# Kernel optimization log

Hardware: AMD Instinct MI355X
Metric: run time of the kernel (lower is better)

Reference implementation:

```python
import jax, jax.numpy as jnp
import numpy as np

B, N, E = 4, 4096, 65536
HID, F_N, F_E, ROUNDS = 128, 32, 16, 3


def setup_inputs() -> dict:
    key = jax.random.key(0)
    ks = jax.random.split(key, 32)
    p = lambda k, shape: 0.02 * jax.random.normal(k, shape, dtype=jnp.float32)
    inp = {
        "nodes": jax.random.normal(ks[0], (B, N, F_N), dtype=jnp.float32),
        "edge_feat": jax.random.normal(ks[1], (B, E, F_E), dtype=jnp.float32),
        "edges": jax.random.randint(ks[2], (B, E, 2), 0, N).astype(jnp.int64),
        "node_mask": jnp.ones((B, N), dtype=bool),
        "edge_mask": jnp.ones((B, E), dtype=bool),
        # projections (stored as (in, out))
        "W_node": p(ks[3], (F_N, HID)),
        "W_edge": p(ks[4], (F_E, HID)),
        "marker": p(ks[5], (HID,)),
        # per-round MLP weights, stacked on leading rounds dim
        "eW1": p(ks[6], (ROUNDS, 3 * HID, HID)),
        "eb1": jnp.zeros((ROUNDS, HID), jnp.float32),
        "eW2": p(ks[7], (ROUNDS, HID, HID)),
        "eb2": jnp.zeros((ROUNDS, HID), jnp.float32),
        "nW1": p(ks[8], (ROUNDS, 2 * HID, HID)),
        "nb1": jnp.zeros((ROUNDS, HID), jnp.float32),
        "nW2": p(ks[9], (ROUNDS, HID, HID)),
        "nb2": jnp.zeros((ROUNDS, HID), jnp.float32),
    }
    return inp


def reference(nodes, edge_feat, edges, node_mask, edge_mask,
              W_node, W_edge, marker, eW1, eb1, eW2, eb2, nW1, nb1, nW2, nb2):
    b, n, _ = nodes.shape
    h = nodes @ W_node                       # (B,N,H)
    ef = edge_feat @ W_edge                  # (B,E,H)
    src = jnp.clip(edges[..., 0], 0, n - 1)  # (B,E)
    dst = jnp.clip(edges[..., 1], 0, n - 1)
    bidx = jnp.arange(b)[:, None]            # (B,1) for batched gather/scatter
    em = edge_mask.astype(h.dtype)[..., None]
    nm = node_mask.astype(h.dtype)[..., None]
    for r in range(ROUNDS):
        h_src = h[bidx, src]                 # (B,E,H) gather
        h_dst = h[bidx, dst]
        cat = jnp.concatenate([h_src, h_dst, ef], axis=-1)   # (B,E,3H)
        msg = jax.nn.silu(cat @ eW1[r] + eb1[r]) @ eW2[r] + eb2[r]
        msg = msg * em
        agg = jnp.zeros_like(h).at[bidx, dst].add(msg)       # scatter-add to nodes
        cat_node = jnp.concatenate([h, agg], axis=-1)        # (B,N,2H)
        upd = jax.nn.silu(cat_node @ nW1[r] + nb1[r]) @ nW2[r] + nb2[r]
        h = (h + upd) * nm
    marker_tok = jnp.broadcast_to(marker[None, None, :], (b, 1, HID))
    return jnp.concatenate([marker_tok, h], axis=1)          # (B,1+N,H)
```

## Files before the change

kernel.cpp:

```cpp
#include <hip/hip_runtime.h>
#include <hip/hip_bf16.h>
#include <cstdint>
#include <cstddef>

#define BB 4
#define NN 4096
#define EE 65536
#define HID 128
#define FN 32
#define FE 16
#define NROUNDS 3

#define XP 168
#define XNP 264
#define PP 136
#define YPITCH 136

typedef __attribute__((ext_vector_type(8))) short short8;
typedef __attribute__((ext_vector_type(4))) float f32x4;
typedef unsigned int uint_t;

__device__ __forceinline__ size_t hrow(int b, int n) {
    return ((size_t)b * (NN + 1) + 1 + n) * HID;
}

__device__ __forceinline__ short f2bf(float f) {
    __hip_bfloat16 h = __float2bfloat16(f);
    return *reinterpret_cast<short*>(&h);
}

__device__ __forceinline__ float bf2f(short s) {
    union { uint32_t u; float f; } v;
    v.u = ((uint32_t)(unsigned short)s) << 16;
    return v.f;
}

__device__ __forceinline__ float bflo(uint_t u) {
    union { uint_t u; float f; } v; v.u = u << 16; return v.f;
}
__device__ __forceinline__ float bfhi(uint_t u) {
    union { uint_t u; float f; } v; v.u = u & 0xFFFF0000u; return v.f;
}

__device__ __forceinline__ float silu(float x) {
    return x * __builtin_amdgcn_rcpf(1.0f + __expf(-x));
}

__device__ __forceinline__ int clipn(int x) {
    return x < 0 ? 0 : (x > NN - 1 ? NN - 1 : x);
}

__global__ void proj_nodes_kernel(const float* __restrict__ nodes,
                                  const float* __restrict__ Wn,
                                  float* __restrict__ hbuf,
                                  short* __restrict__ hbf,
                                  const float* __restrict__ marker,
                                  const float* __restrict__ We,
                                  const float* __restrict__ eW1,
                                  const float* __restrict__ eW2,
                                  const float* __restrict__ nW1,
                                  float* __restrict__ Wec,
                                  float* __restrict__ F,
                                  uint_t* __restrict__ cnt,
                                  uint_t* __restrict__ cntm) {
    __shared__ float nd[8][FN];
    int t = threadIdx.x;
    int row0 = blockIdx.x * 8;

    if (blockIdx.x < 4) {
        hbuf[((size_t)blockIdx.x * (NN + 1)) * HID + t] = marker[t];
    } else if (blockIdx.x < 68) {
        int base = (blockIdx.x - 4) * 256 + t * 2;
        cnt[base] = 0u;  cnt[base + 1] = 0u;
        cntm[base] = 0u; cntm[base + 1] = 0u;
    } else if (blockIdx.x < 116) {
        int lb = blockIdx.x - 68; int r = lb >> 4; int i = lb & 15;
        const float* w1 = eW1 + ((size_t)r * 384 + 256) * HID;
        float acc = 0.f;
        for (int k = 0; k < HID; ++k)
            acc += We[i * HID + k] * w1[k * HID + t];
        Wec[((size_t)r * 16 + i) * HID + t] = acc;
    } else if (blockIdx.x < 500) {
        int lb = blockIdx.x - 116; int r = lb >> 7; int k = lb & 127;
        const float* w2r = eW2 + ((size_t)r * HID + k) * HID;
        const float* n1r = nW1 + ((size_t)r * 256 + 128) * HID;
        float acc = 0.f;
        for (int j = 0; j < HID; ++j)
            acc += w2r[j] * n1r[j * HID + t];
        F[((size_t)r * HID + k) * HID + t] = acc;
    }

    for (int i = 0; i < 2; ++i) {
        int idx = i * 128 + t; int r = idx >> 5; int c = idx & 31;
        nd[r][c] = nodes[(size_t)(row0 + r) * FN + c];
    }
    __syncthreads();
    float acc[8] = {0.f,0.f,0.f,0.f,0.f,0.f,0.f,0.f};
    #pragma unroll
    for (int k = 0; k < FN; ++k) {
        float w = Wn[k * HID + t];
        #pragma unroll
        for (int r = 0; r < 8; ++r) acc[r] += nd[r][k] * w;
    }
    #pragma unroll
    for (int r = 0; r < 8; ++r) {
        int row = row0 + r; int b = row >> 12; int n = row & (NN - 1);
        hbuf[hrow(b, n) + t] = acc[r];
        hbf[(size_t)row * HID + t] = f2bf(acc[r]);
    }
}

__device__ __forceinline__ void pack_generic(const float* __restrict__ W,
                                             short* __restrict__ P,
                                             int KT, size_t rstrideW,
                                             int lb, int lane) {
    int nt = lb & 7;
    int kt = (lb >> 3) % KT;
    int r  = lb / (8 * KT);
    const float* Wr = W + (size_t)r * rstrideW;
    int n  = nt * 16 + (lane & 15);
    int k0 = kt * 32 + (lane >> 4) * 8;
    short v[8];
    #pragma unroll
    for (int i = 0; i < 8; ++i) v[i] = f2bf(Wr[(size_t)(k0 + i) * HID + n]);
    size_t idx = (((size_t)(r * KT + kt) * 8 + nt) * 64 + lane) * 8;
    *(uint4*)&P[idx] = *(uint4*)v;
}

__global__ void pack_all_kernel(const float* __restrict__ eW1,
                                const float* __restrict__ Wec,
                                const float* __restrict__ F,
                                const float* __restrict__ nW1,
                                const float* __restrict__ nW2,
                                const float* __restrict__ eb2,
                                short* __restrict__ W1p,
                                short* __restrict__ eYp,
                                short* __restrict__ nW1p,
                                short* __restrict__ nW2p,
                                float* __restrict__ vecb) {
    int lane = threadIdx.x;
    int bid = blockIdx.x;
    if (bid < 120) {
        const int KT = 5;
        int nt = bid & 7; int kt = (bid >> 3) % KT; int r = bid / (8 * KT);
        int n  = nt * 16 + (lane & 15);
        int k0 = kt * 32 + (lane >> 4) * 8;
        short v[8];
        #pragma unroll
        for (int i = 0; i < 8; ++i) {
            int k = k0 + i;
            float x;
            if (k < 128)      x = eW1[((size_t)r * 384 + k) * HID + n];
            else if (k < 144) x = Wec[((size_t)r * 16 + (k - 128)) * HID + n];
            else              x = 0.f;
            v[i] = f2bf(x);
        }
        size_t idx = (((size_t)(r * KT + kt) * 8 + nt) * 64 + lane) * 8;
        *(uint4*)&W1p[idx] = *(uint4*)v;
    } else if (bid < 216) {
        pack_generic(eW1 + (size_t)128 * HID, eYp, 4, (size_t)384 * HID,
                     bid - 120, lane);
    } else if (bid < 408) {
        const int KT = 8;
        int lb = bid - 216;
        int nt = lb & 7; int kt = (lb >> 3) % KT; int r = lb / (8 * KT);
        int n  = nt * 16 + (lane & 15);
        int k0 = kt * 32 + (lane >> 4) * 8;
        short v[8];
        #pragma unroll
        for (int i = 0; i < 8; ++i) {
            int k = k0 + i;
            float x;
            if (k < 128) x = nW1[((size_t)r * 256 + k) * HID + n];
            else         x = F[((size_t)r * HID + (k - 128)) * HID + n];
            v[i] = f2bf(x);
        }
        size_t idx = (((size_t)(r * KT + kt) * 8 + nt) * 64 + lane) * 8;
        *(uint4*)&nW1p[idx] = *(uint4*)v;
    } else if (bid < 504) {
        pack_generic(nW2, nW2p, 4, (size_t)HID * HID, bid - 408, lane);
    } else {
        int idx = (bid - 504) * 64 + lane;
        int r = idx >> 7; int col = idx & 127;
        const float* n1r = nW1 + ((size_t)r * 256 + 128) * HID;
        float acc = 0.f;
        for (int j = 0; j < HID; ++j)
            acc += eb2[r * HID + j] * n1r[j * HID + col];
        vecb[r * HID + col] = acc;
    }
}

__global__ void hist_kernel(const int* __restrict__ edges,
                            uint_t* __restrict__ cnt) {
    int i = blockIdx.x * 256 + threadIdx.x;
    int b = i >> 16;
    int2 pr = *(const int2*)&edges[(size_t)i * 2];
    int d = clipn(pr.y);
    atomicAdd(&cnt[b * NN + d], 1u);
}

__global__ void scan_kernel(const uint_t* __restrict__ cnt,
                            uint_t* __restrict__ cursor) {
    __shared__ uint_t ps[256];
    int t = threadIdx.x;
    const uint4* c4 = (const uint4*)cnt + (size_t)t * 16;
    uint4 v[16];
    uint_t s = 0;
    #pragma unroll
    for (int i = 0; i < 16; ++i) {
        v[i] = c4[i];
        s += v[i].x + v[i].y + v[i].z + v[i].w;
    }
    ps[t] = s;
    __syncthreads();
    for (int off = 1; off < 256; off <<= 1) {
        uint_t x = (t >= off) ? ps[t - off] : 0u;
        __syncthreads();
        ps[t] += x;
        __syncthreads();
    }
    uint_t run = ps[t] - s;
    uint4* o4 = (uint4*)cursor + (size_t)t * 16;
    #pragma unroll
    for (int i = 0; i < 16; ++i) {
        uint4 o;
        o.x = run;
        o.y = o.x + v[i].x;
        o.z = o.y + v[i].y;
        o.w = o.z + v[i].z;
        run = o.w + v[i].w;
        o4[i] = o;
    }
}

__global__ void scatter_permute_kernel(const int* __restrict__ edges,
                                       const int* __restrict__ emask,
                                       const float* __restrict__ edge_feat,
                                       uint_t* __restrict__ cursor,
                                       uint_t* __restrict__ meta,
                                       short* __restrict__ efs,
                                       uint_t* __restrict__ cntm) {
    int i = blockIdx.x * 256 + threadIdx.x;
    int b = i >> 16;
    int2 pr = *(const int2*)&edges[(size_t)i * 2];
    int s = clipn(pr.x), d = clipn(pr.y);
    uint_t mk = emask[i] ? 1u : 0u;
    if (mk) atomicAdd(&cntm[b * NN + d], 1u);
    uint_t p = atomicAdd(&cursor[b * NN + d], 1u);
    meta[p] = (uint_t)s | ((uint_t)d << 12) | (mk << 24);
    const float* src = edge_feat + (size_t)i * FE;
    short v[16];
    #pragma unroll
    for (int k = 0; k < 16; ++k) v[k] = f2bf(src[k]);
    *(uint4*)(efs + (size_t)p * FE)     = *(uint4*)v;
    *(uint4*)(efs + (size_t)p * FE + 8) = *(uint4*)(v + 8);
}

__global__ __launch_bounds__(256, 6)
void proj_y_kernel(const short* __restrict__ hbf,
                   const short* __restrict__ Wp,
                   const float* __restrict__ b1,
                   short* __restrict__ Y,
                   float* __restrict__ S) {
    __shared__ short X[16 * YPITCH];
    int t = threadIdx.x;
    int row0 = blockIdx.x * 16;

    #pragma unroll
    for (int i = 0; i < 2; ++i) {
        int c = i * 256 + t;
        *(float4*)(S + (size_t)row0 * HID + c * 4) =
            make_float4(0.f, 0.f, 0.f, 0.f);
    }
    {
        int e = t >> 4; int s = t & 15;
        uint4 v = *(const uint4*)(hbf + (size_t)(row0 + e) * HID + s * 8);
        *(uint4*)((char*)X + e * (YPITCH * 2) + s * 16) = v;
    }
    __syncthreads();

    int lane = t & 63;
    int w    = t >> 6;
    int n0 = w * 32;
    int lr = lane & 15;
    int lg = lane >> 4;

    f32x4 acc[2];
    #pragma unroll
    for (int nf = 0; nf < 2; ++nf) {
        float bv = b1[n0 + nf * 16 + lr];
        acc[nf] = (f32x4){bv, bv, bv, bv};
    }
    const char* Xb = (const char*)X;
    for (int kt = 0; kt < 4; ++kt) {
        short8 a = *(const short8*)(Xb + lr * (YPITCH * 2)
                                       + (kt * 32 + lg * 8) * 2);
        const short* wp = Wp + (((size_t)kt * 8 + (n0 >> 4)) * 64 + lane) * 8;
        #pragma unroll
        for (int nf = 0; nf < 2; ++nf) {
            short8 bf = *(const short8*)(wp + (size_t)nf * 64 * 8);
            acc[nf] = __builtin_amdgcn_mfma_f32_16x16x32_bf16(a, bf, acc[nf], 0, 0, 0);
        }
    }
    #pragma unroll
    for (int r = 0; r < 4; ++r) {
        int row = lg * 4 + r;
        #pragma unroll
        for (int nf = 0; nf < 2; ++nf)
            Y[(size_t)(row0 + row) * HID + n0 + nf * 16 + lr]
                = f2bf(acc[nf][r]);
    }
}

__global__ __launch_bounds__(256, 6)
void edge_mfma_csr_kernel(const short* __restrict__ hbf,
                          const short* __restrict__ efs,
                          const uint_t* __restrict__ meta,
                          const short* __restrict__ Y,
                          const short* __restrict__ W1p,
                          float* __restrict__ S) {
    __shared__ short X[64 * XP];
    __shared__ int sdst[64];
    __shared__ float smf[64];
    __shared__ unsigned short segs[65];
    __shared__ int nseg;
    short* Pl = X;

    int t = threadIdx.x;
    int p0 = blockIdx.x * 64;
    int b  = p0 >> 16;

    if (t < 64) {
        uint_t m = meta[p0 + t];
        sdst[t] = (int)((m >> 12) & 0xFFFu);
        smf[t]  = (m >> 24) ? 1.f : 0.f;
        uint_t pm = __shfl_up(m, 1);
        int flag = (t == 0) || (((m ^ pm) & 0x00FFF000u) != 0u);
        unsigned long long mask = __ballot(flag);
        int rank = __popcll(mask & ((1ull << t) - 1ull));
        if (flag) segs[rank] = (unsigned short)t;
        if (t == 0) {
            int ns = __popcll(mask);
            nseg = ns;
            segs[ns] = 64;
        }
    }
    __syncthreads();

    #pragma unroll
    for (int i = 0; i < 4; ++i) {
        int c = i * 256 + t; int e = c >> 4; int s = c & 15;
        int src = (int)(meta[p0 + e] & 0xFFFu);
        uint4 v = *(const uint4*)(hbf + ((size_t)b * NN + src) * HID + s * 8);
        *(uint4*)((char*)X + e * (XP * 2) + s * 16) = v;
    }
    if (t < 128) {
        int e = t >> 1; int s = t & 1;
        uint4 v = *(const uint4*)(efs + (size_t)(p0 + e) * FE + s * 8);
        *(uint4*)((char*)X + e * (XP * 2) + 256 + s * 16) = v;
        *(uint4*)((char*)X + e * (XP * 2) + 288 + s * 16) = make_uint4(0,0,0,0);
    }

    int lane = t & 63;
    int w    = t >> 6;
    int m0 = (w & 1) * 32;
    int n0 = (w >> 1) * 64;
    int lr = lane & 15;
    int lg = lane >> 4;

    f32x4 acc[2][4];
    #pragma unroll
    for (int mf = 0; mf < 2; ++mf)
        #pragma unroll
        for (int r = 0; r < 4; ++r) {
            int row = m0 + mf * 16 + lg * 4 + r;
            const short* yp = Y + ((size_t)b * NN + sdst[row]) * HID + n0 + lr;
            #pragma unroll
            for (int nf = 0; nf < 4; ++nf)
                acc[mf][nf][r] = bf2f(yp[nf * 16]);
        }
    __syncthreads();

    const char* Xb = (const char*)X;
    for (int kt = 0; kt < 5; ++kt) {
        short8 a[2];
        #pragma unroll
        for (int mf = 0; mf < 2; ++mf)
            a[mf] = *(const short8*)(Xb + (m0 + mf * 16 + lr) * (XP * 2)
                                        + (kt * 32 + lg * 8) * 2);
        const short* wp = W1p + (((size_t)kt * 8 + (n0 >> 4)) * 64 + lane) * 8;
        #pragma unroll
        for (int nf = 0; nf < 4; ++nf) {
            short8 bf = *(const short8*)(wp + (size_t)nf * 64 * 8);
            #pragma unroll
            for (int mf = 0; mf < 2; ++mf)
                acc[mf][nf] = __builtin_amdgcn_mfma_f32_16x16x32_bf16(
                    a[mf], bf, acc[mf][nf], 0, 0, 0);
        }
    }
    __syncthreads();

    #pragma unroll
    for (int mf = 0; mf < 2; ++mf)
        #pragma unroll
        for (int nf = 0; nf < 4; ++nf)
            #pragma unroll
            for (int r = 0; r < 4; ++r) {
                int row = m0 + mf * 16 + lg * 4 + r;
                int col = n0 + nf * 16 + lr;
                Pl[row * PP + col] = f2bf(smf[row] * silu(acc[mf][nf][r]));
            }
    __syncthreads();

    {
        int ns = nseg;
        for (int task = t; task < (ns << 6); task += 256) {
            int s  = task >> 6;
            int c2 = (task & 63) * 2;
            int r0 = segs[s], r1 = segs[s + 1];
            float run0 = 0.f, run1 = 0.f;
            for (int r = r0; r < r1; ++r) {
                uint_t pr = *(const uint_t*)&Pl[r * PP + c2];
                run0 += bflo(pr);
                run1 += bfhi(pr);
            }
            float* ap = &S[((size_t)b * NN + sdst[r0]) * HID + c2];
            atomicAdd(ap,     run0);
            atomicAdd(ap + 1, run1);
        }
    }
}

__global__ __launch_bounds__(256, 6)
void node_mfma_kernel(const short* __restrict__ hbf_in,
                      const float* __restrict__ S,
                      const uint_t* __restrict__ cntm,
                      const float* __restrict__ vec,
                      const int* __restrict__ nmask,
                      const short* __restrict__ W1p,
                      const short* __restrict__ W2p,
                      const float* __restrict__ b1,
                      const float* __restrict__ b2,
                      float* __restrict__ hout,
                      short* __restrict__ hbf_out,
                      short* __restrict__ Ynext,
                      const short* __restrict__ eYpN,
                      const float* __restrict__ b1N,
                      float* __restrict__ Sz) {
    __shared__ short X[16 * XNP];
    __shared__ int smk[16];
    __shared__ float scnt[16];
    short* Pl = X;

    int t = threadIdx.x;
    int row0 = blockIdx.x * 16;
    int b  = row0 >> 12;
    int nn0 = row0 & (NN - 1);

    if (t < 16) {
        smk[t]  = nmask[row0 + t];
        scnt[t] = (float)cntm[row0 + t];
    }

    {
        int e = t >> 4; int s = t & 15;
        uint4 v = *(const uint4*)(hbf_in + (size_t)(row0 + e) * HID + s * 8);
        *(uint4*)((char*)X + e * (XNP * 2) + s * 16) = v;
    }
    #pragma unroll
    for (int i = 0; i < 2; ++i) {
        int c = i * 256 + t; int e = c >> 5; int s = c & 31;
        float4 f = *(const float4*)(S + (size_t)(row0 + e) * HID + s * 4);
        short v[4] = { f2bf(f.x), f2bf(f.y), f2bf(f.z), f2bf(f.w) };
        *(uint2*)((char*)X + e * (XNP * 2) + 256 + s * 8) = *(uint2*)v;
    }
    __syncthreads();

    int lane = t & 63;
    int w    = t >> 6;
    int n0 = w * 32;
    int lr = lane & 15;
    int lg = lane >> 4;

    f32x4 acc[2];
    #pragma unroll
    for (int nf = 0; nf < 2; ++nf) {
        int col = n0 + nf * 16 + lr;
        float bv = b1[col];
        float vv = vec[col];
        #pragma unroll
        for (int r = 0; r < 4; ++r)
            acc[nf][r] = bv + scnt[lg * 4 + r] * vv;
    }
    const char* Xb = (const char*)X;
    for (int kt = 0; kt < 8; ++kt) {
        short8 a = *(const short8*)(Xb + lr * (XNP * 2)
                                       + (kt * 32 + lg * 8) * 2);
        const short* wp = W1p + (((size_t)kt * 8 + (n0 >> 4)) * 64 + lane) * 8;
        #pragma unroll
        for (int nf = 0; nf < 2; ++nf) {
            short8 bf = *(const short8*)(wp + (size_t)nf * 64 * 8);
            acc[nf] = __builtin_amdgcn_mfma_f32_16x16x32_bf16(a, bf, acc[nf], 0, 0, 0);
        }
    }
    __syncthreads();

    #pragma unroll
    for (int nf = 0; nf < 2; ++nf)
        #pragma unroll
        for (int r = 0; r < 4; ++r) {
            int row = lg * 4 + r;
            int col = n0 + nf * 16 + lr;
            Pl[row * PP + col] = f2bf(silu(acc[nf][r]));
        }
    __syncthreads();

    f32x4 acc2[2];
    #pragma unroll
    for (int nf = 0; nf < 2; ++nf) {
        float bv = b2[n0 + nf * 16 + lr];
        acc2[nf] = (f32x4){bv, bv, bv, bv};
    }
    const char* Pb = (const char*)Pl;
    for (int kt = 0; kt < 4; ++kt) {
        short8 a = *(const short8*)(Pb + lr * (PP * 2)
                                       + (kt * 32 + lg * 8) * 2);
        const short* wp = W2p + (((size_t)kt * 8 + (n0 >> 4)) * 64 + lane) * 8;
        #pragma unroll
        for (int nf = 0; nf < 2; ++nf) {
            short8 bf = *(const short8*)(wp + (size_t)nf * 64 * 8);
            acc2[nf] = __builtin_amdgcn_mfma_f32_16x16x32_bf16(a, bf, acc2[nf], 0, 0, 0);
        }
    }

    short hn_bf[2][4];
    #pragma unroll
    for (int r = 0; r < 4; ++r) {
        int rl = lg * 4 + r;
        float m = smk[rl] ? 1.f : 0.f;
        size_t ho = hrow(b, nn0 + rl);
        size_t hb = (size_t)(row0 + rl) * HID;
        #pragma unroll
        for (int nf = 0; nf < 2; ++nf) {
            int col = n0 + nf * 16 + lr;
            float hold = hout[ho + col];
            float hn = (hold + acc2[nf][r]) * m;
            hout[ho + col] = hn;
            short hb16 = f2bf(hn);
            hbf_out[hb + col] = hb16;
            hn_bf[nf][r] = hb16;
        }
    }

    if (Ynext == nullptr) return;

    __syncthreads();
    #pragma unroll
    for (int r = 0; r < 4; ++r) {
        int row = lg * 4 + r;
        #pragma unroll
        for (int nf = 0; nf < 2; ++nf)
            Pl[row * PP + n0 + nf * 16 + lr] = hn_bf[nf][r];
    }
    __syncthreads();

    f32x4 accy[2];
    #pragma unroll
    for (int nf = 0; nf < 2; ++nf) {
        float bv = b1N[n0 + nf * 16 + lr];
        accy[nf] = (f32x4){bv, bv, bv, bv};
    }
    for (int kt = 0; kt < 4; ++kt) {
        short8 a = *(const short8*)((const char*)Pl + lr * (PP * 2)
                                       + (kt * 32 + lg * 8) * 2);
        const short* wp = eYpN + (((size_t)kt * 8 + (n0 >> 4)) * 64 + lane) * 8;
        #pragma unroll
        for (int nf = 0; nf < 2; ++nf) {
            short8 bf = *(const short8*)(wp + (size_t)nf * 64 * 8);
            accy[nf] = __builtin_amdgcn_mfma_f32_16x16x32_bf16(a, bf, accy[nf], 0, 0, 0);
        }
    }
    #pragma unroll
    for (int r = 0; r < 4; ++r) {
        int row = lg * 4 + r;
        #pragma unroll
        for (int nf = 0; nf < 2; ++nf)
            Ynext[(size_t)(row0 + row) * HID + n0 + nf * 16 + lr]
                = f2bf(accy[nf][r]);
    }
    #pragma unroll
    for (int i = 0; i < 2; ++i) {
        int c = i * 256 + t;
        *(float4*)(Sz + (size_t)row0 * HID + c * 4) =
            make_float4(0.f, 0.f, 0.f, 0.f);
    }
}

extern "C" void kernel_launch(void* const* d_in, const int* in_sizes, int n_in,
                              void* d_out, int out_size, void* d_ws, size_t ws_size,
                              hipStream_t stream) {
    const float* nodes     = (const float*)d_in[0];
    const float* edge_feat = (const float*)d_in[1];
    const int*   edges     = (const int*)d_in[2];
    const int*   node_mask = (const int*)d_in[3];
    const int*   edge_mask = (const int*)d_in[4];
    const float* W_node    = (const float*)d_in[5];
    const float* W_edge    = (const float*)d_in[6];
    const float* marker    = (const float*)d_in[7];
    const float* eW1       = (const float*)d_in[8];
    const float* eb1       = (const float*)d_in[9];
    const float* eW2       = (const float*)d_in[10];
    const float* eb2       = (const float*)d_in[11];
    const float* nW1       = (const float*)d_in[12];
    const float* nb1       = (const float*)d_in[13];
    const float* nW2       = (const float*)d_in[14];
    const float* nb2       = (const float*)d_in[15];
    float* out = (float*)d_out;

    const size_t HN = (size_t)BB * NN * HID;
    char* wsb = (char*)d_ws;
    float*  S      = (float*)wsb;   wsb += HN * 4;
    short*  hbf    = (short*)wsb;   wsb += HN * 2;
    short*  Yb     = (short*)wsb;   wsb += HN * 2;
    float*  Wec    = (float*)wsb;   wsb += 3 * 16 * HID * 4;
    float*  F      = (float*)wsb;   wsb += 3 * HID * HID * 4;
    float*  vecb   = (float*)wsb;   wsb += 3 * HID * 4;
    short*  W1p    = (short*)wsb;   wsb += 3 * 5 * 4096 * 2;
    short*  eYp    = (short*)wsb;   wsb += 3 * 4 * 4096 * 2;
    short*  nW1p   = (short*)wsb;   wsb += 3 * 8 * 4096 * 2;
    short*  nW2p   = (short*)wsb;   wsb += 3 * 4 * 4096 * 2;
    uint_t* cnt    = (uint_t*)wsb;  wsb += (size_t)BB * NN * 4;
    uint_t* cursor = (uint_t*)wsb;  wsb += (size_t)BB * NN * 4;
    uint_t* cntm   = (uint_t*)wsb;  wsb += (size_t)BB * NN * 4;
    uint_t* meta   = (uint_t*)wsb;  wsb += (size_t)BB * EE * 4;
    short*  efs    = (short*)wsb;   wsb += (size_t)BB * EE * FE * 2;
    if ((size_t)(wsb - (char*)d_ws) > ws_size) return;

    proj_nodes_kernel<<<(BB * NN) / 8, 128, 0, stream>>>(
        nodes, W_node, out, hbf, marker, W_edge, eW1, eW2, nW1,
        Wec, F, cnt, cntm);
    pack_all_kernel<<<510, 64, 0, stream>>>(
        eW1, Wec, F, nW1, nW2, eb2, W1p, eYp, nW1p, nW2p, vecb);
    hist_kernel<<<(BB * EE) / 256, 256, 0, stream>>>(edges, cnt);
    scan_kernel<<<1, 256, 0, stream>>>(cnt, cursor);
    scatter_permute_kernel<<<(BB * EE) / 256, 256, 0, stream>>>(
        edges, edge_mask, edge_feat, cursor, meta, efs, cntm);

    proj_y_kernel<<<(BB * NN) / 16, 256, 0, stream>>>(
        hbf, eYp, eb1, Yb, S);

    for (int r = 0; r < NROUNDS; ++r) {
        edge_mfma_csr_kernel<<<(BB * EE) / 64, 256, 0, stream>>>(
            hbf, efs, meta, Yb,
            W1p + (size_t)r * 5 * 4096,
            S);
        bool last = (r == NROUNDS - 1);
        node_mfma_kernel<<<(BB * NN) / 16, 256, 0, stream>>>(
            hbf, S, cntm, vecb + (size_t)r * HID, node_mask,
            nW1p + (size_t)r * 8 * 4096,
            nW2p + (size_t)r * 4 * 4096,
            nb1 + r * HID,
            nb2 + r * HID,
            out, hbf,
            last ? nullptr : Yb,
            last ? eYp : eYp + (size_t)(r + 1) * 4 * 4096,
            last ? eb1 : eb1 + (size_t)(r + 1) * HID,
            S);
    }
}
```

Baseline: 223.2 us.

## Merge scatter-permute and Y projection kernels; coalesce Y gather in edge kernel

```diff
diff --git a/kernel.cpp b/kernel.cpp
--- a/kernel.cpp
+++ b/kernel.cpp
@@ -233,39 +233,40 @@
     }
 }
 
-__global__ void scatter_permute_kernel(const int* __restrict__ edges,
-                                       const int* __restrict__ emask,
-                                       const float* __restrict__ edge_feat,
-                                       uint_t* __restrict__ cursor,
-                                       uint_t* __restrict__ meta,
-                                       short* __restrict__ efs,
-                                       uint_t* __restrict__ cntm) {
-    int i = blockIdx.x * 256 + threadIdx.x;
-    int b = i >> 16;
-    int2 pr = *(const int2*)&edges[(size_t)i * 2];
-    int s = clipn(pr.x), d = clipn(pr.y);
-    uint_t mk = emask[i] ? 1u : 0u;
-    if (mk) atomicAdd(&cntm[b * NN + d], 1u);
-    uint_t p = atomicAdd(&cursor[b * NN + d], 1u);
-    meta[p] = (uint_t)s | ((uint_t)d << 12) | (mk << 24);
-    const float* src = edge_feat + (size_t)i * FE;
-    short v[16];
-    #pragma unroll
-    for (int k = 0; k < 16; ++k) v[k] = f2bf(src[k]);
-    *(uint4*)(efs + (size_t)p * FE)     = *(uint4*)v;
-    *(uint4*)(efs + (size_t)p * FE + 8) = *(uint4*)(v + 8);
-}
-
-__global__ __launch_bounds__(256, 6)
-void proj_y_kernel(const short* __restrict__ hbf,
-                   const short* __restrict__ Wp,
-                   const float* __restrict__ b1,
-                   short* __restrict__ Y,
-                   float* __restrict__ S) {
+__global__ void scatter_proj_kernel(const int* __restrict__ edges,
+                                    const int* __restrict__ emask,
+                                    const float* __restrict__ edge_feat,
+                                    uint_t* __restrict__ cursor,
+                                    uint_t* __restrict__ meta,
+                                    short* __restrict__ efs,
+                                    uint_t* __restrict__ cntm,
+                                    const short* __restrict__ hbf,
+                                    const short* __restrict__ Wp,
+                                    const float* __restrict__ b1,
+                                    short* __restrict__ Y,
+                                    float* __restrict__ S) {
     __shared__ short X[16 * YPITCH];
     int t = threadIdx.x;
-    int row0 = blockIdx.x * 16;
-
+
+    if (blockIdx.x < 1024) {
+        int i = blockIdx.x * 256 + t;
+        int b = i >> 16;
+        int2 pr = *(const int2*)&edges[(size_t)i * 2];
+        int s = clipn(pr.x), d = clipn(pr.y);
+        uint_t mk = emask[i] ? 1u : 0u;
+        if (mk) atomicAdd(&cntm[b * NN + d], 1u);
+        uint_t p = atomicAdd(&cursor[b * NN + d], 1u);
+        meta[p] = (uint_t)s | ((uint_t)d << 12) | (mk << 24);
+        const float* src = edge_feat + (size_t)i * FE;
+        short v[16];
+        #pragma unroll
+        for (int k = 0; k < 16; ++k) v[k] = f2bf(src[k]);
+        *(uint4*)(efs + (size_t)p * FE)     = *(uint4*)v;
+        *(uint4*)(efs + (size_t)p * FE + 8) = *(uint4*)(v + 8);
+        return;
+    }
+
+    int row0 = (blockIdx.x - 1024) * 16;
     #pragma unroll
     for (int i = 0; i < 2; ++i) {
         int c = i * 256 + t;
@@ -361,6 +362,14 @@
         *(uint4*)((char*)X + e * (XP * 2) + 288 + s * 16) = make_uint4(0,0,0,0);
     }
 
+    uint4 yv[4];
+    #pragma unroll
+    for (int i = 0; i < 4; ++i) {
+        int c = i * 256 + t; int e = c >> 4; int s = c & 15;
+        yv[i] = *(const uint4*)(Y + ((size_t)b * NN + sdst[e]) * HID + s * 8);
+    }
+    __syncthreads();
+
     int lane = t & 63;
     int w    = t >> 6;
     int m0 = (w & 1) * 32;
@@ -372,15 +381,8 @@
     #pragma unroll
     for (int mf = 0; mf < 2; ++mf)
         #pragma unroll
-        for (int r = 0; r < 4; ++r) {
-            int row = m0 + mf * 16 + lg * 4 + r;
-            const short* yp = Y + ((size_t)b * NN + sdst[row]) * HID + n0 + lr;
-            #pragma unroll
-            for (int nf = 0; nf < 4; ++nf)
-                acc[mf][nf][r] = bf2f(yp[nf * 16]);
-        }
-    __syncthreads();
-
+        for (int nf = 0; nf < 4; ++nf)
+            acc[mf][nf] = (f32x4){0.f, 0.f, 0.f, 0.f};
     const char* Xb = (const char*)X;
     for (int kt = 0; kt < 5; ++kt) {
         short8 a[2];
@@ -401,6 +403,13 @@
     __syncthreads();
 
     #pragma unroll
+    for (int i = 0; i < 4; ++i) {
+        int c = i * 256 + t; int e = c >> 4; int s = c & 15;
+        *(uint4*)((char*)Pl + e * (PP * 2) + s * 16) = yv[i];
+    }
+    __syncthreads();
+
+    #pragma unroll
     for (int mf = 0; mf < 2; ++mf)
         #pragma unroll
         for (int nf = 0; nf < 4; ++nf)
@@ -408,7 +417,9 @@
             for (int r = 0; r < 4; ++r) {
                 int row = m0 + mf * 16 + lg * 4 + r;
                 int col = n0 + nf * 16 + lr;
-                Pl[row * PP + col] = f2bf(smf[row] * silu(acc[mf][nf][r]));
+                float y = bf2f(Pl[row * PP + col]);
+                Pl[row * PP + col]
+                    = f2bf(smf[row] * silu(acc[mf][nf][r] + y));
             }
     __syncthreads();
 
@@ -643,10 +654,8 @@
         eW1, Wec, F, nW1, nW2, eb2, W1p, eYp, nW1p, nW2p, vecb);
     hist_kernel<<<(BB * EE) / 256, 256, 0, stream>>>(edges, cnt);
     scan_kernel<<<1, 256, 0, stream>>>(cnt, cursor);
-    scatter_permute_kernel<<<(BB * EE) / 256, 256, 0, stream>>>(
-        edges, edge_mask, edge_feat, cursor, meta, efs, cntm);
-
-    proj_y_kernel<<<(BB * NN) / 16, 256, 0, stream>>>(
+    scatter_proj_kernel<<<2048, 256, 0, stream>>>(
+        edges, edge_mask, edge_feat, cursor, meta, efs, cntm,
         hbf, eYp, eb1, Yb, S);
 
     for (int r = 0; r < NROUNDS; ++r) {
```

New measurement: 245.5 us. +10.0%, slower.
